# Kernel optimization log

Measured on AMD Instinct MI355X. Metric: run time of the kernel, lower is better.

The kernel has to match this reference:

```python
import jax, jax.numpy as jnp
import numpy as np

N, C, W = 16, 512, 4096          # batch lines, channels, max width (frames)
FINAL_DIM = 512
MASK_WIDTH = 4
NUM_NEGATIVES = 10
NUM_MASKS = 256                  # ~ mask_prob * T_total / mask_width


def _build_static():
    # Deterministic ragged lengths, already descending (pack_padded_sequence order).
    seq_len = (W - 128 * np.arange(N)).astype(np.int64)       # [4096, 3968, ..., 2176]
    t = np.arange(W)[:, None]                                  # time-major outer axis
    b = np.arange(N)[None, :]
    valid = seq_len[None, :] > t                               # [W, N]
    # pack_padded_sequence layout: for each t, all batches with len>t (desc length order)
    pack_idx = ((b * W + t)[valid]).astype(np.int64)           # [T_total] indices into flat (N*W)
    T = pack_idx.shape[0]                                      # 50176
    n_blocks = T // MASK_WIDTH
    rng = np.random.default_rng(0)
    perm = rng.permutation(n_blocks)
    sel1 = np.sort(perm[:NUM_MASKS])
    sel2 = np.sort(perm[NUM_MASKS:NUM_MASKS + NUM_NEGATIVES * NUM_MASKS])
    off = np.arange(MASK_WIDTH)
    # non-overlapping contiguous mask_width blocks, ascending (boolean-mask gather order)
    masked_idx = (sel1[:, None] * MASK_WIDTH + off).ravel().astype(np.int64)   # mask == 1
    neg_idx = (sel2[:, None] * MASK_WIDTH + off).ravel().astype(np.int64)      # mask == 2
    return seq_len, pack_idx, masked_idx, neg_idx


def setup_inputs() -> dict:
    key = jax.random.key(0)
    k1, k2, k3 = jax.random.split(key, 3)
    seq_len, pack_idx, masked_idx, neg_idx = _build_static()
    inputs = jax.random.normal(k1, (N, C, 1, W), dtype=jnp.float32)
    mask_emb = jax.random.normal(k2, (MASK_WIDTH, C), dtype=jnp.float32) * 0.02
    Wq = jax.random.normal(k3, (FINAL_DIM, C), dtype=jnp.float32) * (1.0 / np.sqrt(C))
    bq = jnp.zeros((FINAL_DIM,), dtype=jnp.float32)
    return {
        'inputs': inputs,
        'seq_len': jnp.asarray(seq_len, jnp.int32),
        'pack_idx': jnp.asarray(pack_idx, jnp.int32),
        'masked_idx': jnp.asarray(masked_idx, jnp.int32),
        'neg_idx': jnp.asarray(neg_idx, jnp.int32),
        'mask_emb': mask_emb,
        'Wq': Wq,
        'bq': bq,
    }


def reference(inputs, seq_len, pack_idx, masked_idx, neg_idx, mask_emb, Wq, bq):
    Nn, Cc, H, Ww = inputs.shape                              # H == 1
    # (N, C, 1, W) -> (N, W, 1, C) -> flat (N*W, C)
    x = jnp.transpose(inputs, (0, 3, 2, 1)).reshape(Nn * Ww, Cc)
    packed = x[pack_idx]                                      # [T_total, C] packed (time-major)
    # project_q on masked (mask==1) and negative (mask==2) token groups
    unmasked = (packed[masked_idx] @ Wq.T + bq).reshape(1, NUM_MASKS, MASK_WIDTH, FINAL_DIM)
    negatives = (packed[neg_idx] @ Wq.T + bq).reshape(NUM_NEGATIVES, NUM_MASKS, MASK_WIDTH, FINAL_DIM)
    # overwrite masked positions with the repeated mask embedding table
    packed = packed.at[masked_idx].set(jnp.tile(mask_emb, (NUM_MASKS, 1)))
    # pad_packed_sequence: scatter back to padded (N, W, C), zeros elsewhere
    out = jnp.zeros((Nn * Ww, Cc), dtype=inputs.dtype).at[pack_idx].set(packed)
    out = out.reshape(Nn, Ww, Cc).transpose(0, 2, 1)[:, :, None, :]   # (N, C, 1, W)
    return out, unmasked, negatives
```

## Files before the change

kernel.cpp:

```cpp
#include <hip/hip_runtime.h>

#define NB 16
#define CC 512
#define WW 4096
#define FD 512
#define NMASK 1024
#define T_COMB 11264
#define OUT0_ELEMS (NB*CC*WW)

#define WS_LOOKUP_OFF 0
#define WS_WQ_OFF     262144
#define WS_A_OFF      786432

#define S_LDS 36

typedef __attribute__((ext_vector_type(8))) short short8;
typedef __attribute__((ext_vector_type(4))) float f32x4;

__device__ __forceinline__ unsigned short f2bf(float x) {
  unsigned int u = __builtin_bit_cast(unsigned int, x);
  u += 0x7fffu + ((u >> 16) & 1u);
  return (unsigned short)(u >> 16);
}

__device__ __forceinline__ void gload_lds16(const void* gp, void* lp) {
  __builtin_amdgcn_global_load_lds(
      (__attribute__((address_space(1))) void*)(gp),
      (__attribute__((address_space(3))) void*)(lp),
      16, 0, 0);
}

__global__ __launch_bounds__(256) void scatter_lookup_k(
    const int* __restrict__ pack_idx, const int* __restrict__ masked_idx,
    const int* __restrict__ neg_idx, int* __restrict__ lookup) {
  int g = blockIdx.x * 256 + threadIdx.x;
  int pidx = (g < NMASK) ? masked_idx[g] : neg_idx[g - NMASK];
  lookup[pack_idx[pidx]] = g;
}

__global__ __launch_bounds__(256) void fused_copy_k(
    const float* __restrict__ in, const int* __restrict__ seq_len,
    const int* __restrict__ lookup, const float* __restrict__ mask_emb,
    const float* __restrict__ Wq, float* __restrict__ out0,
    unsigned short* __restrict__ A_ws, unsigned short* __restrict__ Wq_ws) {
  if (blockIdx.x >= 2048) {
    int b2 = blockIdx.x - 2048;
    const float4* wq4 = (const float4*)Wq;
#pragma unroll
    for (int it = 0; it < 4; ++it) {
      int i4 = it * 16384 + b2 * 256 + (int)threadIdx.x;
      float4 v = wq4[i4];
      ushort4 o;
      o.x = f2bf(v.x); o.y = f2bf(v.y); o.z = f2bf(v.z); o.w = f2bf(v.w);
      ((ushort4*)Wq_ws)[i4] = o;
    }
    return;
  }
  const int tid = threadIdx.x;
  const int bx = blockIdx.x;
  const int n = bx >> 7;
  const int w0 = (bx & 127) * 32;
  const int wl4 = (tid & 7) * 4;
  const int w = w0 + wl4;
  const int c0 = tid >> 3;
  const size_t rowbase = ((size_t)n << 21) + (size_t)w;
  float4* out4 = (float4*)out0;
  const int L = seq_len[n];

  if (w0 + 32 > L) {
    float4 z = {0.f, 0.f, 0.f, 0.f};
#pragma unroll
    for (int it = 0; it < 16; ++it) {
      int c = it * 32 + c0;
      out4[(rowbase + ((size_t)c << 12)) >> 2] = z;
    }
    return;
  }

  __shared__ unsigned short tile[CC * S_LDS];
  __shared__ int g_s[32];
  if (tid < 32) g_s[tid] = lookup[n * WW + w0 + tid];

  const int4 g4 = *(const int4*)&lookup[n * WW + w];
  const int gg[4] = {g4.x, g4.y, g4.z, g4.w};
  bool lane_has_mask = ((unsigned)gg[0] < (unsigned)NMASK) |
                       ((unsigned)gg[1] < (unsigned)NMASK) |
                       ((unsigned)gg[2] < (unsigned)NMASK) |
                       ((unsigned)gg[3] < (unsigned)NMASK);
  bool has_mask = __ballot(lane_has_mask) != 0ull;

  const float4* in4 = (const float4*)in;
#pragma unroll
  for (int it = 0; it < 16; ++it) {
    int c = it * 32 + c0;
    size_t i4 = (rowbase + ((size_t)c << 12)) >> 2;
    float4 v = in4[i4];
    ushort4 bf;
    bf.x = f2bf(v.x); bf.y = f2bf(v.y); bf.z = f2bf(v.z); bf.w = f2bf(v.w);
    *(ushort4*)&tile[c * S_LDS + wl4] = bf;
    if (has_mask) {
      float o[4] = {v.x, v.y, v.z, v.w};
#pragma unroll
      for (int k = 0; k < 4; ++k)
        if ((unsigned)gg[k] < (unsigned)NMASK)
          o[k] = mask_emb[(gg[k] & 3) * CC + c];
      v.x = o[0]; v.y = o[1]; v.z = o[2]; v.w = o[3];
    }
    out4[i4] = v;
  }
  __syncthreads();

  const int lane = tid & 63;
  bool sel = (lane < 32) && (g_s[lane & 31] >= 0);
  unsigned smask = (unsigned)__ballot(sel);
  const int c2 = tid * 2;
  while (smask) {
    int wl = __builtin_ctz(smask);
    smask &= smask - 1;
    int g = g_s[wl];
    ushort2 val;
    val.x = tile[c2 * S_LDS + wl];
    val.y = tile[(c2 + 1) * S_LDS + wl];
    *(ushort2*)&A_ws[(size_t)g * CC + c2] = val;
  }
}

__global__ __launch_bounds__(256) void gemm_k(
    const unsigned short* __restrict__ A, const unsigned short* __restrict__ B,
    const float* __restrict__ bq, float* __restrict__ out) {
  __shared__ unsigned short As[64 * 32];
  __shared__ unsigned short Bs[128 * 32];
  const int tid = threadIdx.x;
  const int lane = tid & 63;
  const int quad = lane >> 4;
  const int r16 = lane & 15;
  const int wv = tid >> 6;
  const int bm = blockIdx.x * 64;
  const int bf = blockIdx.y * 128;
  const int wm = (wv & 1) * 32;
  const int wf = (wv >> 1) * 64;
  const int wbase = tid & ~63;

  f32x4 acc[2][4];
#pragma unroll
  for (int mi = 0; mi < 2; ++mi)
#pragma unroll
    for (int fi = 0; fi < 4; ++fi)
      acc[mi][fi] = (f32x4){0.f, 0.f, 0.f, 0.f};

  for (int k0 = 0; k0 < 512; k0 += 32) {
    {
      int row = tid >> 2, cg = tid & 3;
      gload_lds16(A + (size_t)(bm + row) * 512 + k0 + cg * 8, &As[wbase * 8]);
    }
#pragma unroll
    for (int it = 0; it < 2; ++it) {
      int ch = it * 256 + tid;
      int row = ch >> 2, cg = ch & 3;
      gload_lds16(B + (size_t)(bf + row) * 512 + k0 + cg * 8,
                  &Bs[(it * 256 + wbase) * 8]);
    }
    asm volatile("s_waitcnt vmcnt(0)" ::: "memory");
    __syncthreads();

    short8 a[2], b[4];
#pragma unroll
    for (int mi = 0; mi < 2; ++mi)
      a[mi] = *(const short8*)&As[(wm + mi * 16 + r16) * 32 + quad * 8];
#pragma unroll
    for (int fi = 0; fi < 4; ++fi)
      b[fi] = *(const short8*)&Bs[(wf + fi * 16 + r16) * 32 + quad * 8];
#pragma unroll
    for (int mi = 0; mi < 2; ++mi)
#pragma unroll
      for (int fi = 0; fi < 4; ++fi)
        acc[mi][fi] = __builtin_amdgcn_mfma_f32_16x16x32_bf16(
            a[mi], b[fi], acc[mi][fi], 0, 0, 0);
    __syncthreads();
  }

#pragma unroll
  for (int fi = 0; fi < 4; ++fi) {
    int f = bf + wf + fi * 16 + r16;
    float bqv = bq[f];
#pragma unroll
    for (int mi = 0; mi < 2; ++mi) {
      int m0 = bm + wm + mi * 16 + quad * 4;
#pragma unroll
      for (int r = 0; r < 4; ++r)
        out[(size_t)(m0 + r) * 512 + f] = acc[mi][fi][r] + bqv;
    }
  }
}

extern "C" void kernel_launch(void* const* d_in, const int* in_sizes, int n_in,
                              void* d_out, int out_size, void* d_ws, size_t ws_size,
                              hipStream_t stream) {
  const float* inputs    = (const float*)d_in[0];
  const int*   seq_len   = (const int*)d_in[1];
  const int*   pack_idx  = (const int*)d_in[2];
  const int*   masked_idx= (const int*)d_in[3];
  const int*   neg_idx   = (const int*)d_in[4];
  const float* mask_emb  = (const float*)d_in[5];
  const float* Wq        = (const float*)d_in[6];
  const float* bq        = (const float*)d_in[7];
  float* out = (float*)d_out;
  char* ws = (char*)d_ws;
  int* lookup = (int*)(ws + WS_LOOKUP_OFF);
  unsigned short* wqb = (unsigned short*)(ws + WS_WQ_OFF);
  unsigned short* aws = (unsigned short*)(ws + WS_A_OFF);

  hipMemsetAsync(lookup, 0xFF, NB * WW * sizeof(int), stream);
  scatter_lookup_k<<<44, 256, 0, stream>>>(pack_idx, masked_idx, neg_idx, lookup);
  fused_copy_k<<<2112, 256, 0, stream>>>(inputs, seq_len, lookup, mask_emb, Wq,
                                         out, aws, wqb);
  gemm_k<<<dim3(176, 4), 256, 0, stream>>>(aws, wqb, bq, out + OUT0_ELEMS);
}
```

Before: 296.1 us.

## Halve copy-kernel LDS tile, shrink GEMM tile, merge Wq conversion into prep

The Wq-to-bf16 conversion moves from the tail of the copy kernel into the lookup-scatter kernel, giving the copy kernel a uniform 2048-block grid. The copy kernel now stages channels in two halves through a 256-row LDS tile, which halves its shared memory to allow more resident blocks, at the cost of an extra barrier and a second scatter pass. The GEMM tile shrinks from 64x128 to 64x64 and gets an occupancy hint, doubling the grid so more CUs are busy, at the cost of more redundant A loads.

```diff
diff --git a/kernel.cpp b/kernel.cpp
--- a/kernel.cpp
+++ b/kernel.cpp
@@ -3,7 +3,6 @@
 #define NB 16
 #define CC 512
 #define WW 4096
-#define FD 512
 #define NMASK 1024
 #define T_COMB 11264
 #define OUT0_ELEMS (NB*CC*WW)
@@ -30,21 +29,17 @@
       16, 0, 0);
 }
 
-__global__ __launch_bounds__(256) void scatter_lookup_k(
+__global__ __launch_bounds__(256) void prep_k(
     const int* __restrict__ pack_idx, const int* __restrict__ masked_idx,
-    const int* __restrict__ neg_idx, int* __restrict__ lookup) {
-  int g = blockIdx.x * 256 + threadIdx.x;
-  int pidx = (g < NMASK) ? masked_idx[g] : neg_idx[g - NMASK];
-  lookup[pack_idx[pidx]] = g;
-}
-
-__global__ __launch_bounds__(256) void fused_copy_k(
-    const float* __restrict__ in, const int* __restrict__ seq_len,
-    const int* __restrict__ lookup, const float* __restrict__ mask_emb,
-    const float* __restrict__ Wq, float* __restrict__ out0,
-    unsigned short* __restrict__ A_ws, unsigned short* __restrict__ Wq_ws) {
-  if (blockIdx.x >= 2048) {
-    int b2 = blockIdx.x - 2048;
+    const int* __restrict__ neg_idx, int* __restrict__ lookup,
+    const float* __restrict__ Wq, unsigned short* __restrict__ Wq_ws) {
+  int b = blockIdx.x;
+  if (b < 44) {
+    int g = b * 256 + (int)threadIdx.x;
+    int pidx = (g < NMASK) ? masked_idx[g] : neg_idx[g - NMASK];
+    lookup[pack_idx[pidx]] = g;
+  } else {
+    int b2 = b - 44;
     const float4* wq4 = (const float4*)Wq;
 #pragma unroll
     for (int it = 0; it < 4; ++it) {
@@ -54,8 +49,13 @@
       o.x = f2bf(v.x); o.y = f2bf(v.y); o.z = f2bf(v.z); o.w = f2bf(v.w);
       ((ushort4*)Wq_ws)[i4] = o;
     }
-    return;
-  }
+  }
+}
+
+__global__ __launch_bounds__(256) void fused_copy_k(
+    const float* __restrict__ in, const int* __restrict__ seq_len,
+    const int* __restrict__ lookup, const float* __restrict__ mask_emb,
+    float* __restrict__ out0, unsigned short* __restrict__ A_ws) {
   const int tid = threadIdx.x;
   const int bx = blockIdx.x;
   const int n = bx >> 7;
@@ -77,7 +77,7 @@
     return;
   }
 
-  __shared__ unsigned short tile[CC * S_LDS];
+  __shared__ unsigned short tile[256 * S_LDS];
   __shared__ int g_s[32];
   if (tid < 32) g_s[tid] = lookup[n * WW + w0 + tid];
 
@@ -90,97 +90,93 @@
   bool has_mask = __ballot(lane_has_mask) != 0ull;
 
   const float4* in4 = (const float4*)in;
-#pragma unroll
-  for (int it = 0; it < 16; ++it) {
-    int c = it * 32 + c0;
-    size_t i4 = (rowbase + ((size_t)c << 12)) >> 2;
-    float4 v = in4[i4];
-    ushort4 bf;
-    bf.x = f2bf(v.x); bf.y = f2bf(v.y); bf.z = f2bf(v.z); bf.w = f2bf(v.w);
-    *(ushort4*)&tile[c * S_LDS + wl4] = bf;
-    if (has_mask) {
-      float o[4] = {v.x, v.y, v.z, v.w};
-#pragma unroll
-      for (int k = 0; k < 4; ++k)
-        if ((unsigned)gg[k] < (unsigned)NMASK)
-          o[k] = mask_emb[(gg[k] & 3) * CC + c];
-      v.x = o[0]; v.y = o[1]; v.z = o[2]; v.w = o[3];
-    }
-    out4[i4] = v;
-  }
-  __syncthreads();
-
-  const int lane = tid & 63;
-  bool sel = (lane < 32) && (g_s[lane & 31] >= 0);
-  unsigned smask = (unsigned)__ballot(sel);
-  const int c2 = tid * 2;
-  while (smask) {
-    int wl = __builtin_ctz(smask);
-    smask &= smask - 1;
-    int g = g_s[wl];
-    ushort2 val;
-    val.x = tile[c2 * S_LDS + wl];
-    val.y = tile[(c2 + 1) * S_LDS + wl];
-    *(ushort2*)&A_ws[(size_t)g * CC + c2] = val;
-  }
-}
-
-__global__ __launch_bounds__(256) void gemm_k(
+  unsigned smask = 0;
+#pragma unroll
+  for (int half = 0; half < 2; ++half) {
+    const int cbase = half << 8;
+#pragma unroll
+    for (int it = 0; it < 8; ++it) {
+      int c = cbase + it * 32 + c0;
+      size_t i4 = (rowbase + ((size_t)c << 12)) >> 2;
+      float4 v = in4[i4];
+      ushort4 bf;
+      bf.x = f2bf(v.x); bf.y = f2bf(v.y); bf.z = f2bf(v.z); bf.w = f2bf(v.w);
+      *(ushort4*)&tile[(c - cbase) * S_LDS + wl4] = bf;
+      if (has_mask) {
+        float o[4] = {v.x, v.y, v.z, v.w};
+#pragma unroll
+        for (int k = 0; k < 4; ++k)
+          if ((unsigned)gg[k] < (unsigned)NMASK)
+            o[k] = mask_emb[(gg[k] & 3) * CC + c];
+        v.x = o[0]; v.y = o[1]; v.z = o[2]; v.w = o[3];
+      }
+      out4[i4] = v;
+    }
+    __syncthreads();
+    if (half == 0) {
+      const int lane = tid & 63;
+      bool sel = (lane < 32) && (g_s[lane] >= 0);
+      smask = (unsigned)__ballot(sel);
+    }
+    unsigned m = smask;
+    while (m) {
+      int wl = __builtin_ctz(m);
+      m &= m - 1;
+      int g = g_s[wl];
+      A_ws[(size_t)g * CC + cbase + tid] = tile[tid * S_LDS + wl];
+    }
+    if (half == 0) __syncthreads();
+  }
+}
+
+__global__ __launch_bounds__(256, 8) void gemm_k(
     const unsigned short* __restrict__ A, const unsigned short* __restrict__ B,
     const float* __restrict__ bq, float* __restrict__ out) {
   __shared__ unsigned short As[64 * 32];
-  __shared__ unsigned short Bs[128 * 32];
+  __shared__ unsigned short Bs[64 * 32];
   const int tid = threadIdx.x;
   const int lane = tid & 63;
   const int quad = lane >> 4;
   const int r16 = lane & 15;
   const int wv = tid >> 6;
   const int bm = blockIdx.x * 64;
-  const int bf = blockIdx.y * 128;
+  const int bf = blockIdx.y * 64;
   const int wm = (wv & 1) * 32;
-  const int wf = (wv >> 1) * 64;
+  const int wf = (wv >> 1) * 32;
   const int wbase = tid & ~63;
-
-  f32x4 acc[2][4];
+  const int row = tid >> 2, cg = tid & 3;
+
+  f32x4 acc[2][2];
 #pragma unroll
   for (int mi = 0; mi < 2; ++mi)
 #pragma unroll
-    for (int fi = 0; fi < 4; ++fi)
+    for (int fi = 0; fi < 2; ++fi)
       acc[mi][fi] = (f32x4){0.f, 0.f, 0.f, 0.f};
 
   for (int k0 = 0; k0 < 512; k0 += 32) {
-    {
-      int row = tid >> 2, cg = tid & 3;
-      gload_lds16(A + (size_t)(bm + row) * 512 + k0 + cg * 8, &As[wbase * 8]);
-    }
-#pragma unroll
-    for (int it = 0; it < 2; ++it) {
-      int ch = it * 256 + tid;
-      int row = ch >> 2, cg = ch & 3;
-      gload_lds16(B + (size_t)(bf + row) * 512 + k0 + cg * 8,
-                  &Bs[(it * 256 + wbase) * 8]);
-    }
+    gload_lds16(A + (size_t)(bm + row) * 512 + k0 + cg * 8, &As[wbase * 8]);
+    gload_lds16(B + (size_t)(bf + row) * 512 + k0 + cg * 8, &Bs[wbase * 8]);
     asm volatile("s_waitcnt vmcnt(0)" ::: "memory");
     __syncthreads();
 
-    short8 a[2], b[4];
+    short8 a[2], b[2];
 #pragma unroll
     for (int mi = 0; mi < 2; ++mi)
       a[mi] = *(const short8*)&As[(wm + mi * 16 + r16) * 32 + quad * 8];
 #pragma unroll
-    for (int fi = 0; fi < 4; ++fi)
+    for (int fi = 0; fi < 2; ++fi)
       b[fi] = *(const short8*)&Bs[(wf + fi * 16 + r16) * 32 + quad * 8];
 #pragma unroll
     for (int mi = 0; mi < 2; ++mi)
 #pragma unroll
-      for (int fi = 0; fi < 4; ++fi)
+      for (int fi = 0; fi < 2; ++fi)
         acc[mi][fi] = __builtin_amdgcn_mfma_f32_16x16x32_bf16(
             a[mi], b[fi], acc[mi][fi], 0, 0, 0);
     __syncthreads();
   }
 
 #pragma unroll
-  for (int fi = 0; fi < 4; ++fi) {
+  for (int fi = 0; fi < 2; ++fi) {
     int f = bf + wf + fi * 16 + r16;
     float bqv = bq[f];
 #pragma unroll
@@ -211,8 +207,8 @@
   unsigned short* aws = (unsigned short*)(ws + WS_A_OFF);
 
   hipMemsetAsync(lookup, 0xFF, NB * WW * sizeof(int), stream);
-  scatter_lookup_k<<<44, 256, 0, stream>>>(pack_idx, masked_idx, neg_idx, lookup);
-  fused_copy_k<<<2112, 256, 0, stream>>>(inputs, seq_len, lookup, mask_emb, Wq,
-                                         out, aws, wqb);
-  gemm_k<<<dim3(176, 4), 256, 0, stream>>>(aws, wqb, bq, out + OUT0_ELEMS);
-}
+  prep_k<<<108, 256, 0, stream>>>(pack_idx, masked_idx, neg_idx, lookup, Wq, wqb);
+  fused_copy_k<<<2048, 256, 0, stream>>>(inputs, seq_len, lookup, mask_emb,
+                                         out, aws);
+  gemm_k<<<dim3(176, 8), 256, 0, stream>>>(aws, wqb, bq, out + OUT0_ELEMS);
+}
```

After: 314.3 us. +6.1%, slower.
